# Performance work log

Measured on AMD Instinct MI355X. Metric: run time of the kernel, lower is better.

Reference implementation:

```python
import jax, jax.numpy as jnp
import numpy as np

N = 50000       # nodes per protein graph
E = 400000      # directed edges per graph (before self-loops)
H = 4           # attention heads
C = 64          # per-head output channels (output_dim)
OUT = 64        # fc output dim
NEG_SLOPE_ATT = 0.2   # PyG GATConv default negative_slope
NEG_SLOPE_ACT = 0.01  # nn.LeakyReLU default


def gat_conv(x, edge_index, W, a_src, a_dst, b):
    """PyG GATConv (concat=True, add_self_loops=True), eval mode (no dropout).
    x: [N, F_in]; edge_index: [2, E] int (row 0 = src, row 1 = dst).
    W: [F_in, H*C]; a_src, a_dst: [H, C]; b: [H*C].
    """
    n = x.shape[0]
    h = (x @ W).reshape(n, H, C)                      # [N, H, C]
    loops = jnp.arange(n, dtype=edge_index.dtype)
    src = jnp.concatenate([edge_index[0], loops])     # [E+N]
    dst = jnp.concatenate([edge_index[1], loops])
    asrc = jnp.einsum('nhc,hc->nh', h, a_src)         # [N, H]
    adst = jnp.einsum('nhc,hc->nh', h, a_dst)
    logits = jax.nn.leaky_relu(asrc[src] + adst[dst], NEG_SLOPE_ATT)  # [E+N, H]
    # scatter-softmax over incoming edges of each dst node
    m = jax.ops.segment_max(logits, dst, num_segments=n)
    m = jnp.where(jnp.isfinite(m), m, 0.0)
    e = jnp.exp(logits - m[dst])
    denom = jax.ops.segment_sum(e, dst, num_segments=n)
    alpha = e / (denom[dst] + 1e-16)                  # [E+N, H]
    out = jax.ops.segment_sum(h[src] * alpha[:, :, None], dst, num_segments=n)  # [N, H, C]
    return out.reshape(n, H * C) + b


def setup_inputs() -> dict:
    key = jax.random.key(0)
    ks = jax.random.split(key, 20)
    d = {
        'x1': jax.random.normal(ks[0], (N, 1), jnp.float32),
        'edge_index1': jax.random.randint(ks[1], (2, E), 0, N, jnp.int32),
        'edge_attr1': jax.random.normal(ks[2], (E, 1), jnp.float32),
        'x2': jax.random.normal(ks[3], (N, 1), jnp.float32),
        'edge_index2': jax.random.randint(ks[4], (2, E), 0, N, jnp.int32),
        'edge_attr2': jax.random.normal(ks[5], (E, 1), jnp.float32),
    }
    s = 0.1
    d['WA'] = jax.random.normal(ks[6], (1, H * C), jnp.float32) * s
    d['a_srcA'] = jax.random.normal(ks[7], (H, C), jnp.float32) * s
    d['a_dstA'] = jax.random.normal(ks[8], (H, C), jnp.float32) * s
    d['bA'] = jnp.zeros((H * C,), jnp.float32)
    d['WB'] = jax.random.normal(ks[9], (1, H * C), jnp.float32) * s
    d['a_srcB'] = jax.random.normal(ks[10], (H, C), jnp.float32) * s
    d['a_dstB'] = jax.random.normal(ks[11], (H, C), jnp.float32) * s
    d['bB'] = jnp.zeros((H * C,), jnp.float32)
    d['fcW'] = jax.random.normal(ks[12], (H * C, OUT), jnp.float32) * s
    d['fcb'] = jnp.zeros((OUT,), jnp.float32)
    return d


def reference(x1, edge_index1, edge_attr1, x2, edge_index2, edge_attr2,
              WA, a_srcA, a_dstA, bA, WB, a_srcB, a_dstB, bB, fcW, fcb):
    # edge_attr is passed but GATConv was built without edge_dim -> ignored by PyG.
    # dropout layers are identity in eval mode.
    h1 = jax.nn.leaky_relu(gat_conv(x1, edge_index1, WA, a_srcA, a_dstA, bA), NEG_SLOPE_ACT)
    h2 = jax.nn.leaky_relu(gat_conv(x2, edge_index2, WB, a_srcB, a_dstB, bB), NEG_SLOPE_ACT)
    return (h1 @ fcW + fcb, h2 @ fcW + fcb)
```

## Files before the change

kernel.cpp:

```cpp
#include <hip/hip_runtime.h>
#include <math.h>
#include <stdint.h>

typedef unsigned int u32;
typedef float f4 __attribute__((ext_vector_type(4)));

#define BSH    7
#define BSZ    128
#define SB     128
#define CAPB   1536
#define SLOT   28
#define SSTR   29
#define SPILL  64
#define ST     1024
#define EPT    4
#define AT     512
#define NBFMAX 512


__global__ __launch_bounds__(ST) void k_place(
    const int* __restrict__ ei1, const float* __restrict__ x1,
    const int* __restrict__ ei2, const float* __restrict__ x2,
    const float* __restrict__ WA, const float* __restrict__ asA,
    const float* __restrict__ adA, const float* __restrict__ bA,
    const float* __restrict__ WB, const float* __restrict__ asB,
    const float* __restrict__ adB, const float* __restrict__ bB,
    const float* __restrict__ fcW,
    float* __restrict__ ws, u32* __restrict__ q, int* __restrict__ cursor,
    int E, int NBF, int CH) {
  const int g   = blockIdx.y;
  const int blk = blockIdx.x;
  const int*   ei = g ? ei2 : ei1;
  const float* x  = g ? x2  : x1;

  __shared__ int lofs[NBFMAX];
  __shared__ int sbase[NBFMAX];
  const int tid = threadIdx.x;
  for (int i = tid; i < NBF; i += ST) lofs[i] = 0;
  __syncthreads();

  const int e0 = blk * CH;
  const int e1 = min(e0 + CH, E);
  u32 pk[EPT];
  int bb[EPT], pp[EPT];
  #pragma unroll
  for (int j = 0; j < EPT; ++j) {
    int e = e0 + j * ST + tid;
    bb[j] = -1;
    if (e < e1) {
      int s = ei[e], d = ei[E + e];
      _Float16 hf = (_Float16)x[s];
      u32 hb = (u32)__builtin_bit_cast(unsigned short, hf);
      pk[j] = (hb << 16) | (u32)d;
      bb[j] = d >> BSH;
      pp[j] = atomicAdd(&lofs[bb[j]], 1);
    }
  }
  __syncthreads();
  for (int b = tid; b < NBF; b += ST) {
    int c = lofs[b];
    sbase[b] = c ? atomicAdd(&cursor[g * NBF + b], c) : 0;
  }
  __syncthreads();
  #pragma unroll
  for (int j = 0; j < EPT; ++j) {
    if (bb[j] >= 0) {
      int idx = sbase[bb[j]] + pp[j];
      if (idx < CAPB) q[((size_t)g * NBF + bb[j]) * CAPB + idx] = pk[j];
    }
  }

  if (blk == 0) {
    const float* W  = g ? WB : WA;
    const float* as = g ? asB : asA;
    const float* ad = g ? adB : adA;
    const float* bw = g ? bB  : bA;
    __shared__ float red[4];
    if (tid < 256) {
      float w0 = W[tid];
      float vs = w0 * as[tid], vd = w0 * ad[tid], vb = fabsf(bw[tid]);
      #pragma unroll
      for (int off = 32; off > 0; off >>= 1) {
        vs += __shfl_down(vs, off, 64);
        vd += __shfl_down(vd, off, 64);
        vb += __shfl_down(vb, off, 64);
      }
      if ((tid & 63) == 0) {
        int h = tid >> 6;
        ws[g * 8 + h] = vs; ws[g * 8 + 4 + h] = vd; red[h] = vb;
      }
    }
    __syncthreads();
    if (tid == 0) ws[16 + g] = red[0] + red[1] + red[2] + red[3];
    if (tid < 256) {
      int h = tid >> 6, k = tid & 63;
      float accp = 0.f, accq = 0.f;
      #pragma unroll 8
      for (int c = 0; c < 64; ++c) {
        float wv = W[h * 64 + c];
        float f  = fcW[(h * 64 + c) * 64 + k];
        accp += wv * f;
        accq += fabsf(wv) * f;
      }
      ws[32 + g * 256 + tid]  = accp;
      ws[544 + g * 256 + tid] = accq;
    }
  }
}

__global__ __launch_bounds__(AT) void k_accum_out(
    const u32* __restrict__ q, const int* __restrict__ cursor,
    const float* __restrict__ x1, const float* __restrict__ x2,
    const float* __restrict__ ws,
    const float* __restrict__ WA, const float* __restrict__ bA,
    const float* __restrict__ WB, const float* __restrict__ bB,
    const float* __restrict__ fcW, const float* __restrict__ fcb,
    float* __restrict__ out, int N, int NBF) {
  const int g = blockIdx.y;
  const int b = blockIdx.x;
  const float* x = g ? x2 : x1;
  const int lo = b << BSH;
  const int nr = min(N - lo, BSZ);
  if (nr <= 0) return;

  __shared__ u32 slots[BSZ * SSTR];
  __shared__ int scur[BSZ];
  __shared__ float sx[BSZ];
  __shared__ float sS[BSZ * 4];
  __shared__ float ss8[8];
  __shared__ u32 sspill[SPILL];
  __shared__ int spill_n;
  __shared__ float sP[256], sQ[256], sfcb[64];
  const int tid = threadIdx.x;
  for (int i = tid; i < BSZ; i += AT) scur[i] = 0;
  for (int i = tid; i < nr; i += AT) sx[i] = x[lo + i];
  for (int i = tid; i < 256; i += AT) { sP[i] = ws[32 + g*256 + i]; sQ[i] = ws[544 + g*256 + i]; }
  if (tid < 64) sfcb[tid] = fcb[tid];
  if (tid < 8)  ss8[tid] = ws[g * 8 + tid];
  if (tid == 0) spill_n = 0;
  const float flag = ws[16] + ws[17];
  const int cnt = min(cursor[g * NBF + b], CAPB);
  const u32* stripe = q + ((size_t)g * NBF + b) * CAPB;
  __syncthreads();

  for (int i = tid; i < cnt; i += AT) {
    u32 u = stripe[i];
    int rel = (int)(u & 0xFFFFu) - lo;
    int pos = atomicAdd(&scur[rel], 1);
    if (pos < SLOT) slots[rel * SSTR + pos] = u;
    else { int sp = atomicAdd(&spill_n, 1); if (sp < SPILL) sspill[sp] = u; }
  }
  __syncthreads();

  const int sn = min(spill_n, SPILL);
  for (int i = tid; i < nr * 4; i += AT) {
    int n = i >> 2, h = i & 3;
    float sh = ss8[h], dh = ss8[4 + h];
    float xd = sx[n];
    float xdd = xd * dh;
    float den = 0.f, num = 0.f;
    int c = min(scur[n], SLOT);
    int base = n * SSTR;
    for (int j = 0; j < c; ++j) {
      u32 u = slots[base + j];
      float xs = (float)__builtin_bit_cast(_Float16, (unsigned short)(u >> 16));
      float l = fmaf(xs, sh, xdd);
      l = (l > 0.f) ? l : 0.2f * l;
      float w = __expf(l);
      den += w;
      num += w * xs;
    }
    for (int j = 0; j < sn; ++j) {
      u32 u = sspill[j];
      if ((int)(u & 0xFFFFu) - lo == n) {
        float xs = (float)__builtin_bit_cast(_Float16, (unsigned short)(u >> 16));
        float l = fmaf(xs, sh, xdd);
        l = (l > 0.f) ? l : 0.2f * l;
        float w = __expf(l);
        den += w;
        num += w * xs;
      }
    }
    float l = xd * (sh + dh);
    l = (l > 0.f) ? l : 0.2f * l;
    float w = __expf(l);
    sS[n * 4 + h] = (num + w * xd) / (den + w + 1e-16f);
  }
  __syncthreads();

  float* ogf = out + ((size_t)g * N + lo) * 64;
  if (flag == 0.0f) {
    f4* og = (f4*)ogf;
    for (int i = tid; i < nr * 16; i += AT) {
      int n = i >> 4, k = (i & 15) * 4;
      float S0 = sS[n*4], S1 = sS[n*4+1], S2 = sS[n*4+2], S3 = sS[n*4+3];
      float A0 = fabsf(S0), A1 = fabsf(S1), A2 = fabsf(S2), A3 = fabsf(S3);
      f4 r;
      r.x = sfcb[k]   + 0.505f*(S0*sP[k]   + S1*sP[64+k] + S2*sP[128+k] + S3*sP[192+k])
                      + 0.495f*(A0*sQ[k]   + A1*sQ[64+k] + A2*sQ[128+k] + A3*sQ[192+k]);
      r.y = sfcb[k+1] + 0.505f*(S0*sP[k+1] + S1*sP[65+k] + S2*sP[129+k] + S3*sP[193+k])
                      + 0.495f*(A0*sQ[k+1] + A1*sQ[65+k] + A2*sQ[129+k] + A3*sQ[193+k]);
      r.z = sfcb[k+2] + 0.505f*(S0*sP[k+2] + S1*sP[66+k] + S2*sP[130+k] + S3*sP[194+k])
                      + 0.495f*(A0*sQ[k+2] + A1*sQ[66+k] + A2*sQ[130+k] + A3*sQ[194+k]);
      r.w = sfcb[k+3] + 0.505f*(S0*sP[k+3] + S1*sP[67+k] + S2*sP[131+k] + S3*sP[195+k])
                      + 0.495f*(A0*sQ[k+3] + A1*sQ[67+k] + A2*sQ[131+k] + A3*sQ[195+k]);
      __builtin_nontemporal_store(r, &og[i]);
    }
  } else {
    const float* W = g ? WB : WA;
    const float* bw = g ? bB : bA;
    for (int i = tid; i < nr * 64; i += AT) {
      int n = i >> 6, k = i & 63;
      float S0 = sS[n*4], S1 = sS[n*4+1], S2 = sS[n*4+2], S3 = sS[n*4+3];
      float y = sfcb[k];
      for (int c = 0; c < 64; ++c) {
        float z0 = S0 * W[c]       + bw[c];
        float z1 = S1 * W[64 + c]  + bw[64 + c];
        float z2 = S2 * W[128 + c] + bw[128 + c];
        float z3 = S3 * W[192 + c] + bw[192 + c];
        z0 = (z0 > 0.f) ? z0 : 0.01f * z0;
        z1 = (z1 > 0.f) ? z1 : 0.01f * z1;
        z2 = (z2 > 0.f) ? z2 : 0.01f * z2;
        z3 = (z3 > 0.f) ? z3 : 0.01f * z3;
        y += z0 * fcW[c * 64 + k] + z1 * fcW[(64 + c) * 64 + k]
           + z2 * fcW[(128 + c) * 64 + k] + z3 * fcW[(192 + c) * 64 + k];
      }
      ogf[(size_t)n * 64 + k] = y;
    }
  }
}

extern "C" void kernel_launch(void* const* d_in, const int* in_sizes, int n_in,
                              void* d_out, int out_size, void* d_ws, size_t ws_size,
                              hipStream_t stream) {
  const float* x1  = (const float*)d_in[0];
  const int*   ei1 = (const int*)  d_in[1];
  const float* x2  = (const float*)d_in[3];
  const int*   ei2 = (const int*)  d_in[4];
  const float* WA  = (const float*)d_in[6];
  const float* asA = (const float*)d_in[7];
  const float* adA = (const float*)d_in[8];
  const float* bA  = (const float*)d_in[9];
  const float* WB  = (const float*)d_in[10];
  const float* asB = (const float*)d_in[11];
  const float* adB = (const float*)d_in[12];
  const float* bB  = (const float*)d_in[13];
  const float* fcW = (const float*)d_in[14];
  const float* fcb = (const float*)d_in[15];
  float* out = (float*)d_out;
  float* ws  = (float*)d_ws;

  const int N   = in_sizes[0];
  const int E   = in_sizes[1] / 2;
  const int NBF = (N + BSZ - 1) >> BSH;
  const int CH  = (E + SB - 1) / SB;

  int* cursor = (int*)(ws + 2048);
  u32* q      = (u32*)(ws + 4096);

  (void)hipMemsetAsync(cursor, 0, (size_t)2 * NBF * sizeof(int), stream);
  k_place<<<dim3(SB, 2), ST, 0, stream>>>(
      ei1, x1, ei2, x2, WA, asA, adA, bA, WB, asB, adB, bB, fcW,
      ws, q, cursor, E, NBF, CH);
  k_accum_out<<<dim3(NBF, 2), AT, 0, stream>>>(
      q, cursor, x1, x2, ws,
      WA, bA, WB, bB, fcW, fcb, out, N, NBF);
}
```

Measured before the change: 35.12 us.

## Fuse memset, placement and accumulation into one cooperative kernel with grid syncs

Replaces the cursor memset and the two separate kernels with a single cooperative launch. Grid-wide syncs separate three phases: zeroing the cursors and precomputing weights, bucketing edges, and per-bucket softmax aggregation plus the output projection. Destination buckets grow from 128 to 256 nodes. Edges are first staged in shared-memory cells per bucket so the global queue writes are grouped, and a persistent loop walks the buckets. This removes launch gaps and the memset, but adds grid-sync cost and leaves load imbalance, since 392 bucket tiles run on 256 blocks.

```diff
diff --git a/kernel.cpp b/kernel.cpp
--- a/kernel.cpp
+++ b/kernel.cpp
@@ -1,81 +1,62 @@
 #include <hip/hip_runtime.h>
+#include <hip/hip_cooperative_groups.h>
 #include <math.h>
 #include <stdint.h>
 
+namespace cg = cooperative_groups;
+
 typedef unsigned int u32;
 typedef float f4 __attribute__((ext_vector_type(4)));
 
-#define BSH    7
-#define BSZ    128
-#define SB     128
-#define CAPB   1536
+#define BSH    8
+#define BSZ    256
+#define NBFMAX 256
+#define SBG    128
+#define GRID   256
+#define NT     1024
+#define CELL   32
+#define CAPB   2688
 #define SLOT   28
 #define SSTR   29
 #define SPILL  64
-#define ST     1024
 #define EPT    4
-#define AT     512
-#define NBFMAX 512
-
-
-__global__ __launch_bounds__(ST) void k_place(
-    const int* __restrict__ ei1, const float* __restrict__ x1,
-    const int* __restrict__ ei2, const float* __restrict__ x2,
-    const float* __restrict__ WA, const float* __restrict__ asA,
-    const float* __restrict__ adA, const float* __restrict__ bA,
-    const float* __restrict__ WB, const float* __restrict__ asB,
-    const float* __restrict__ adB, const float* __restrict__ bB,
-    const float* __restrict__ fcW,
-    float* __restrict__ ws, u32* __restrict__ q, int* __restrict__ cursor,
-    int E, int NBF, int CH) {
-  const int g   = blockIdx.y;
+
+struct PlaceSh {
+  u32 cells[NBFMAX * CELL];
+  int lofs[NBFMAX];
+  int sbase[NBFMAX];
+};
+struct AccSh {
+  u32 slots[BSZ * SSTR];
+  int scur[BSZ];
+  float sx[BSZ];
+  float sS[BSZ * 4];
+  float sP[256], sQ[256], sfcb[64];
+  u32 sspill[SPILL];
+  int spill_n;
+};
+
+
+__global__ __launch_bounds__(NT) void k_fused(
+    const int* ei1, const float* x1, const int* ei2, const float* x2,
+    const float* WA, const float* asA, const float* adA, const float* bA,
+    const float* WB, const float* asB, const float* adB, const float* bB,
+    const float* fcW, const float* fcb,
+    float* ws, u32* q, int* cursor, float* out,
+    int N, int E, int NBF, int CH) {
+  cg::grid_group grid = cg::this_grid();
+  __shared__ union { PlaceSh p; AccSh a; } sh;
+  __shared__ float red[4];
+  const int tid = threadIdx.x;
   const int blk = blockIdx.x;
-  const int*   ei = g ? ei2 : ei1;
-  const float* x  = g ? x2  : x1;
-
-  __shared__ int lofs[NBFMAX];
-  __shared__ int sbase[NBFMAX];
-  const int tid = threadIdx.x;
-  for (int i = tid; i < NBF; i += ST) lofs[i] = 0;
-  __syncthreads();
-
-  const int e0 = blk * CH;
-  const int e1 = min(e0 + CH, E);
-  u32 pk[EPT];
-  int bb[EPT], pp[EPT];
-  #pragma unroll
-  for (int j = 0; j < EPT; ++j) {
-    int e = e0 + j * ST + tid;
-    bb[j] = -1;
-    if (e < e1) {
-      int s = ei[e], d = ei[E + e];
-      _Float16 hf = (_Float16)x[s];
-      u32 hb = (u32)__builtin_bit_cast(unsigned short, hf);
-      pk[j] = (hb << 16) | (u32)d;
-      bb[j] = d >> BSH;
-      pp[j] = atomicAdd(&lofs[bb[j]], 1);
-    }
-  }
-  __syncthreads();
-  for (int b = tid; b < NBF; b += ST) {
-    int c = lofs[b];
-    sbase[b] = c ? atomicAdd(&cursor[g * NBF + b], c) : 0;
-  }
-  __syncthreads();
-  #pragma unroll
-  for (int j = 0; j < EPT; ++j) {
-    if (bb[j] >= 0) {
-      int idx = sbase[bb[j]] + pp[j];
-      if (idx < CAPB) q[((size_t)g * NBF + bb[j]) * CAPB + idx] = pk[j];
-    }
-  }
-
-  if (blk == 0) {
+
+  for (int i = blk * NT + tid; i < 2 * NBF; i += GRID * NT) cursor[i] = 0;
+  if (blk < 2) {
+    const int g = blk;
     const float* W  = g ? WB : WA;
     const float* as = g ? asB : asA;
     const float* ad = g ? adB : adA;
     const float* bw = g ? bB  : bA;
-    __shared__ float red[4];
     if (tid < 256) {
       float w0 = W[tid];
       float vs = w0 * as[tid], vd = w0 * ad[tid], vb = fabsf(bw[tid]);
@@ -106,137 +87,171 @@
       ws[544 + g * 256 + tid] = accq;
     }
   }
-}
-
-__global__ __launch_bounds__(AT) void k_accum_out(
-    const u32* __restrict__ q, const int* __restrict__ cursor,
-    const float* __restrict__ x1, const float* __restrict__ x2,
-    const float* __restrict__ ws,
-    const float* __restrict__ WA, const float* __restrict__ bA,
-    const float* __restrict__ WB, const float* __restrict__ bB,
-    const float* __restrict__ fcW, const float* __restrict__ fcb,
-    float* __restrict__ out, int N, int NBF) {
-  const int g = blockIdx.y;
-  const int b = blockIdx.x;
-  const float* x = g ? x2 : x1;
-  const int lo = b << BSH;
-  const int nr = min(N - lo, BSZ);
-  if (nr <= 0) return;
-
-  __shared__ u32 slots[BSZ * SSTR];
-  __shared__ int scur[BSZ];
-  __shared__ float sx[BSZ];
-  __shared__ float sS[BSZ * 4];
-  __shared__ float ss8[8];
-  __shared__ u32 sspill[SPILL];
-  __shared__ int spill_n;
-  __shared__ float sP[256], sQ[256], sfcb[64];
-  const int tid = threadIdx.x;
-  for (int i = tid; i < BSZ; i += AT) scur[i] = 0;
-  for (int i = tid; i < nr; i += AT) sx[i] = x[lo + i];
-  for (int i = tid; i < 256; i += AT) { sP[i] = ws[32 + g*256 + i]; sQ[i] = ws[544 + g*256 + i]; }
-  if (tid < 64) sfcb[tid] = fcb[tid];
-  if (tid < 8)  ss8[tid] = ws[g * 8 + tid];
-  if (tid == 0) spill_n = 0;
+  grid.sync();
+
+  {
+    const int g = blk >> 7;
+    const int chunk = blk & 127;
+    const int* ei = g ? ei2 : ei1;
+    const float* x = g ? x2 : x1;
+    for (int i = tid; i < NBF; i += NT) sh.p.lofs[i] = 0;
+    __syncthreads();
+    const int e0 = chunk * CH;
+    const int e1 = min(e0 + CH, E);
+    u32 pk[EPT]; int bb[EPT], pp[EPT];
+    #pragma unroll
+    for (int j = 0; j < EPT; ++j) {
+      int e = e0 + j * NT + tid;
+      bb[j] = -1;
+      if (e < e1) {
+        int s = ei[e], d = ei[E + e];
+        _Float16 hf = (_Float16)x[s];
+        u32 hb = (u32)__builtin_bit_cast(unsigned short, hf);
+        pk[j] = (hb << 16) | (u32)d;
+        bb[j] = d >> BSH;
+        pp[j] = atomicAdd(&sh.p.lofs[bb[j]], 1);
+        if (pp[j] < CELL) sh.p.cells[bb[j] * CELL + pp[j]] = pk[j];
+      }
+    }
+    __syncthreads();
+    for (int b = tid; b < NBF; b += NT) {
+      int c = sh.p.lofs[b];
+      sh.p.sbase[b] = c ? atomicAdd(&cursor[g * NBF + b], c) : 0;
+    }
+    __syncthreads();
+    u32* const qg = q + (size_t)g * NBF * CAPB;
+    for (int i = tid; i < NBF * CELL; i += NT) {
+      int b = i >> 5, j = i & (CELL - 1);
+      if (j < min(sh.p.lofs[b], CELL)) {
+        int idx = sh.p.sbase[b] + j;
+        if (idx < CAPB) qg[(size_t)b * CAPB + idx] = sh.p.cells[i];
+      }
+    }
+    #pragma unroll
+    for (int j = 0; j < EPT; ++j) {
+      if (bb[j] >= 0 && pp[j] >= CELL) {
+        int idx = sh.p.sbase[bb[j]] + pp[j];
+        if (idx < CAPB) qg[(size_t)bb[j] * CAPB + idx] = pk[j];
+      }
+    }
+  }
+  grid.sync();
+
   const float flag = ws[16] + ws[17];
-  const int cnt = min(cursor[g * NBF + b], CAPB);
-  const u32* stripe = q + ((size_t)g * NBF + b) * CAPB;
-  __syncthreads();
-
-  for (int i = tid; i < cnt; i += AT) {
-    u32 u = stripe[i];
-    int rel = (int)(u & 0xFFFFu) - lo;
-    int pos = atomicAdd(&scur[rel], 1);
-    if (pos < SLOT) slots[rel * SSTR + pos] = u;
-    else { int sp = atomicAdd(&spill_n, 1); if (sp < SPILL) sspill[sp] = u; }
-  }
-  __syncthreads();
-
-  const int sn = min(spill_n, SPILL);
-  for (int i = tid; i < nr * 4; i += AT) {
-    int n = i >> 2, h = i & 3;
-    float sh = ss8[h], dh = ss8[4 + h];
-    float xd = sx[n];
-    float xdd = xd * dh;
-    float den = 0.f, num = 0.f;
-    int c = min(scur[n], SLOT);
-    int base = n * SSTR;
-    for (int j = 0; j < c; ++j) {
-      u32 u = slots[base + j];
-      float xs = (float)__builtin_bit_cast(_Float16, (unsigned short)(u >> 16));
-      float l = fmaf(xs, sh, xdd);
-      l = (l > 0.f) ? l : 0.2f * l;
-      float w = __expf(l);
-      den += w;
-      num += w * xs;
-    }
-    for (int j = 0; j < sn; ++j) {
-      u32 u = sspill[j];
-      if ((int)(u & 0xFFFFu) - lo == n) {
-        float xs = (float)__builtin_bit_cast(_Float16, (unsigned short)(u >> 16));
-        float l = fmaf(xs, sh, xdd);
+  for (int t = blk; t < 2 * NBF; t += GRID) {
+    const int g = t >= NBF ? 1 : 0;
+    const int b = t - g * NBF;
+    const float* x = g ? x2 : x1;
+    const int lo = b << BSH;
+    const int nr = min(N - lo, BSZ);
+    if (nr > 0) {
+      for (int i = tid; i < BSZ; i += NT) sh.a.scur[i] = 0;
+      for (int i = tid; i < nr; i += NT) sh.a.sx[i] = x[lo + i];
+      for (int i = tid; i < 256; i += NT) { sh.a.sP[i] = ws[32 + g*256 + i]; sh.a.sQ[i] = ws[544 + g*256 + i]; }
+      if (tid < 64) sh.a.sfcb[tid] = fcb[tid];
+      if (tid == 0) sh.a.spill_n = 0;
+      float s8r[8];
+      #pragma unroll
+      for (int j2 = 0; j2 < 8; ++j2) s8r[j2] = ws[g * 8 + j2];
+      const int cnt = min(cursor[g * NBF + b], CAPB);
+      const u32* stripe = q + ((size_t)g * NBF + b) * CAPB;
+      __syncthreads();
+
+      for (int i = tid; i < cnt; i += NT) {
+        u32 u = stripe[i];
+        int rel = (int)(u & 0xFFFFu) - lo;
+        int pos = atomicAdd(&sh.a.scur[rel], 1);
+        if (pos < SLOT) sh.a.slots[rel * SSTR + pos] = u;
+        else { int sp = atomicAdd(&sh.a.spill_n, 1); if (sp < SPILL) sh.a.sspill[sp] = u; }
+      }
+      __syncthreads();
+
+      const int sn = min(sh.a.spill_n, SPILL);
+      for (int i = tid; i < nr * 4; i += NT) {
+        int n = i >> 2, h = i & 3;
+        float shh = s8r[h], dh = s8r[4 + h];
+        float xd = sh.a.sx[n];
+        float xdd = xd * dh;
+        float den = 0.f, num = 0.f;
+        int c = min(sh.a.scur[n], SLOT);
+        int base = n * SSTR;
+        for (int j = 0; j < c; ++j) {
+          u32 u = sh.a.slots[base + j];
+          float xs = (float)__builtin_bit_cast(_Float16, (unsigned short)(u >> 16));
+          float l = fmaf(xs, shh, xdd);
+          l = (l > 0.f) ? l : 0.2f * l;
+          float w = __expf(l);
+          den += w; num += w * xs;
+        }
+        for (int j = 0; j < sn; ++j) {
+          u32 u = sh.a.sspill[j];
+          if ((int)(u & 0xFFFFu) - lo == n) {
+            float xs = (float)__builtin_bit_cast(_Float16, (unsigned short)(u >> 16));
+            float l = fmaf(xs, shh, xdd);
+            l = (l > 0.f) ? l : 0.2f * l;
+            float w = __expf(l);
+            den += w; num += w * xs;
+          }
+        }
+        float l = xd * (shh + dh);
         l = (l > 0.f) ? l : 0.2f * l;
         float w = __expf(l);
-        den += w;
-        num += w * xs;
-      }
-    }
-    float l = xd * (sh + dh);
-    l = (l > 0.f) ? l : 0.2f * l;
-    float w = __expf(l);
-    sS[n * 4 + h] = (num + w * xd) / (den + w + 1e-16f);
-  }
-  __syncthreads();
-
-  float* ogf = out + ((size_t)g * N + lo) * 64;
-  if (flag == 0.0f) {
-    f4* og = (f4*)ogf;
-    for (int i = tid; i < nr * 16; i += AT) {
-      int n = i >> 4, k = (i & 15) * 4;
-      float S0 = sS[n*4], S1 = sS[n*4+1], S2 = sS[n*4+2], S3 = sS[n*4+3];
-      float A0 = fabsf(S0), A1 = fabsf(S1), A2 = fabsf(S2), A3 = fabsf(S3);
-      f4 r;
-      r.x = sfcb[k]   + 0.505f*(S0*sP[k]   + S1*sP[64+k] + S2*sP[128+k] + S3*sP[192+k])
-                      + 0.495f*(A0*sQ[k]   + A1*sQ[64+k] + A2*sQ[128+k] + A3*sQ[192+k]);
-      r.y = sfcb[k+1] + 0.505f*(S0*sP[k+1] + S1*sP[65+k] + S2*sP[129+k] + S3*sP[193+k])
-                      + 0.495f*(A0*sQ[k+1] + A1*sQ[65+k] + A2*sQ[129+k] + A3*sQ[193+k]);
-      r.z = sfcb[k+2] + 0.505f*(S0*sP[k+2] + S1*sP[66+k] + S2*sP[130+k] + S3*sP[194+k])
-                      + 0.495f*(A0*sQ[k+2] + A1*sQ[66+k] + A2*sQ[130+k] + A3*sQ[194+k]);
-      r.w = sfcb[k+3] + 0.505f*(S0*sP[k+3] + S1*sP[67+k] + S2*sP[131+k] + S3*sP[195+k])
-                      + 0.495f*(A0*sQ[k+3] + A1*sQ[67+k] + A2*sQ[131+k] + A3*sQ[195+k]);
-      __builtin_nontemporal_store(r, &og[i]);
-    }
-  } else {
-    const float* W = g ? WB : WA;
-    const float* bw = g ? bB : bA;
-    for (int i = tid; i < nr * 64; i += AT) {
-      int n = i >> 6, k = i & 63;
-      float S0 = sS[n*4], S1 = sS[n*4+1], S2 = sS[n*4+2], S3 = sS[n*4+3];
-      float y = sfcb[k];
-      for (int c = 0; c < 64; ++c) {
-        float z0 = S0 * W[c]       + bw[c];
-        float z1 = S1 * W[64 + c]  + bw[64 + c];
-        float z2 = S2 * W[128 + c] + bw[128 + c];
-        float z3 = S3 * W[192 + c] + bw[192 + c];
-        z0 = (z0 > 0.f) ? z0 : 0.01f * z0;
-        z1 = (z1 > 0.f) ? z1 : 0.01f * z1;
-        z2 = (z2 > 0.f) ? z2 : 0.01f * z2;
-        z3 = (z3 > 0.f) ? z3 : 0.01f * z3;
-        y += z0 * fcW[c * 64 + k] + z1 * fcW[(64 + c) * 64 + k]
-           + z2 * fcW[(128 + c) * 64 + k] + z3 * fcW[(192 + c) * 64 + k];
-      }
-      ogf[(size_t)n * 64 + k] = y;
-    }
+        sh.a.sS[n * 4 + h] = (num + w * xd) / (den + w + 1e-16f);
+      }
+      __syncthreads();
+
+      float* ogf = out + ((size_t)g * N + lo) * 64;
+      if (flag == 0.0f) {
+        f4* og = (f4*)ogf;
+        for (int i = tid; i < nr * 16; i += NT) {
+          int n = i >> 4, k = (i & 15) * 4;
+          float S0 = sh.a.sS[n*4], S1 = sh.a.sS[n*4+1], S2 = sh.a.sS[n*4+2], S3 = sh.a.sS[n*4+3];
+          float A0 = fabsf(S0), A1 = fabsf(S1), A2 = fabsf(S2), A3 = fabsf(S3);
+          f4 r;
+          r.x = sh.a.sfcb[k]   + 0.505f*(S0*sh.a.sP[k]   + S1*sh.a.sP[64+k] + S2*sh.a.sP[128+k] + S3*sh.a.sP[192+k])
+                               + 0.495f*(A0*sh.a.sQ[k]   + A1*sh.a.sQ[64+k] + A2*sh.a.sQ[128+k] + A3*sh.a.sQ[192+k]);
+          r.y = sh.a.sfcb[k+1] + 0.505f*(S0*sh.a.sP[k+1] + S1*sh.a.sP[65+k] + S2*sh.a.sP[129+k] + S3*sh.a.sP[193+k])
+                               + 0.495f*(A0*sh.a.sQ[k+1] + A1*sh.a.sQ[65+k] + A2*sh.a.sQ[129+k] + A3*sh.a.sQ[193+k]);
+          r.z = sh.a.sfcb[k+2] + 0.505f*(S0*sh.a.sP[k+2] + S1*sh.a.sP[66+k] + S2*sh.a.sP[130+k] + S3*sh.a.sP[194+k])
+                               + 0.495f*(A0*sh.a.sQ[k+2] + A1*sh.a.sQ[66+k] + A2*sh.a.sQ[130+k] + A3*sh.a.sQ[194+k]);
+          r.w = sh.a.sfcb[k+3] + 0.505f*(S0*sh.a.sP[k+3] + S1*sh.a.sP[67+k] + S2*sh.a.sP[131+k] + S3*sh.a.sP[195+k])
+                               + 0.495f*(A0*sh.a.sQ[k+3] + A1*sh.a.sQ[67+k] + A2*sh.a.sQ[131+k] + A3*sh.a.sQ[195+k]);
+          __builtin_nontemporal_store(r, &og[i]);
+        }
+      } else {
+        const float* W = g ? WB : WA;
+        const float* bw = g ? bB : bA;
+        for (int i = tid; i < nr * 64; i += NT) {
+          int n = i >> 6, k = i & 63;
+          float S0 = sh.a.sS[n*4], S1 = sh.a.sS[n*4+1], S2 = sh.a.sS[n*4+2], S3 = sh.a.sS[n*4+3];
+          float y = sh.a.sfcb[k];
+          for (int c = 0; c < 64; ++c) {
+            float z0 = S0 * W[c]       + bw[c];
+            float z1 = S1 * W[64 + c]  + bw[64 + c];
+            float z2 = S2 * W[128 + c] + bw[128 + c];
+            float z3 = S3 * W[192 + c] + bw[192 + c];
+            z0 = (z0 > 0.f) ? z0 : 0.01f * z0;
+            z1 = (z1 > 0.f) ? z1 : 0.01f * z1;
+            z2 = (z2 > 0.f) ? z2 : 0.01f * z2;
+            z3 = (z3 > 0.f) ? z3 : 0.01f * z3;
+            y += z0 * fcW[c * 64 + k] + z1 * fcW[(64 + c) * 64 + k]
+               + z2 * fcW[(128 + c) * 64 + k] + z3 * fcW[(192 + c) * 64 + k];
+          }
+          ogf[(size_t)n * 64 + k] = y;
+        }
+      }
+    }
+    __syncthreads();
   }
 }
 
 extern "C" void kernel_launch(void* const* d_in, const int* in_sizes, int n_in,
                               void* d_out, int out_size, void* d_ws, size_t ws_size,
                               hipStream_t stream) {
+  const int*   ei1 = (const int*)  d_in[1];
   const float* x1  = (const float*)d_in[0];
-  const int*   ei1 = (const int*)  d_in[1];
+  const int*   ei2 = (const int*)  d_in[4];
   const float* x2  = (const float*)d_in[3];
-  const int*   ei2 = (const int*)  d_in[4];
   const float* WA  = (const float*)d_in[6];
   const float* asA = (const float*)d_in[7];
   const float* adA = (const float*)d_in[8];
@@ -250,19 +265,20 @@
   float* out = (float*)d_out;
   float* ws  = (float*)d_ws;
 
-  const int N   = in_sizes[0];
-  const int E   = in_sizes[1] / 2;
-  const int NBF = (N + BSZ - 1) >> BSH;
-  const int CH  = (E + SB - 1) / SB;
+  int N   = in_sizes[0];
+  int E   = in_sizes[1] / 2;
+  int NBF = (N + BSZ - 1) >> BSH;
+  int CH  = (E + SBG - 1) / SBG;
 
   int* cursor = (int*)(ws + 2048);
   u32* q      = (u32*)(ws + 4096);
 
-  (void)hipMemsetAsync(cursor, 0, (size_t)2 * NBF * sizeof(int), stream);
-  k_place<<<dim3(SB, 2), ST, 0, stream>>>(
-      ei1, x1, ei2, x2, WA, asA, adA, bA, WB, asB, adB, bB, fcW,
-      ws, q, cursor, E, NBF, CH);
-  k_accum_out<<<dim3(NBF, 2), AT, 0, stream>>>(
-      q, cursor, x1, x2, ws,
-      WA, bA, WB, bB, fcW, fcb, out, N, NBF);
+  void* args[] = { (void*)&ei1, (void*)&x1, (void*)&ei2, (void*)&x2,
+                   (void*)&WA, (void*)&asA, (void*)&adA, (void*)&bA,
+                   (void*)&WB, (void*)&asB, (void*)&adB, (void*)&bB,
+                   (void*)&fcW, (void*)&fcb,
+                   (void*)&ws, (void*)&q, (void*)&cursor, (void*)&out,
+                   (void*)&N, (void*)&E, (void*)&NBF, (void*)&CH };
+  (void)hipLaunchCooperativeKernel((const void*)k_fused, dim3(GRID), dim3(NT),
+                                   args, 0u, stream);
 }
```

New measurement: 95.44 us. 172% more time.
